# Optimization experiments

Measured on AMD Instinct MI355X. Metric: run time of the kernel, lower is better.

Reference implementation:

```python
import jax, jax.numpy as jnp
import numpy as np

B, S, D_IN, D_OUT, RANK, HBS, ABS = 4, 2048, 4096, 4096, 32, 128, 16


def _hadamard(n: int) -> np.ndarray:
    H = np.array([[1.0]], dtype=np.float64)
    while H.shape[0] < n:
        H = np.block([[H, H], [H, -H]])
    return (H / np.sqrt(n)).astype(np.float32)


def setup_inputs() -> dict:
    key = jax.random.key(0)
    ks = jax.random.split(key, 6)
    x = jax.random.normal(ks[0], (B, S, D_IN), dtype=jnp.float32)
    # random +/-1 sign vector (matches torch.randint(0,2)*2-1)
    S_in = (jax.random.randint(ks[1], (D_IN,), 0, 2) * 2 - 1).astype(jnp.float32)
    H_block = jnp.asarray(_hadamard(HBS))  # orthonormal block Hadamard
    w_quantized = jax.random.normal(ks[2], (D_OUT, D_IN), dtype=jnp.float32) * 0.02
    lora_a = jax.random.normal(ks[3], (RANK, D_IN), dtype=jnp.float32) * 0.01
    lora_b = jax.random.normal(ks[4], (D_OUT, RANK), dtype=jnp.float32) * 0.01
    bias = jax.random.normal(ks[5], (D_OUT,), dtype=jnp.float32) * 0.01
    return {"x": x, "S_in": S_in, "H_block": H_block, "w_quantized": w_quantized,
            "lora_a": lora_a, "lora_b": lora_b, "bias": bias}


def _quantize_nvfp4(x, block_size=ABS):
    # per-block (size 16) NVFP4 fake-quant; numel here is divisible by block_size
    levels = jnp.array([0.0, 0.5, 1.0, 1.5, 2.0, 3.0, 4.0, 6.0], dtype=x.dtype)
    shape = x.shape
    xf = x.reshape(-1, block_size)
    amax = jnp.maximum(jnp.max(jnp.abs(xf), axis=-1, keepdims=True), 1e-12)
    scale = amax / 6.0
    x_norm = jnp.abs(xf) / scale
    idx = jnp.argmin(jnp.abs(x_norm[..., None] - levels), axis=-1)  # snap to grid
    xq = jnp.sign(xf) * levels[idx] * scale
    return xq.reshape(shape)


def _hadamard_rotate(x, S_in, H_block):
    # sign flip then block-diagonal Hadamard on the last dim
    shape = x.shape
    x_s = x * S_in
    x3 = x_s.reshape(*shape[:-1], shape[-1] // HBS, HBS)
    return (x3 @ H_block).reshape(shape)


def reference(x, S_in, H_block, w_quantized, lora_a, lora_b, bias):
    x_rot = _hadamard_rotate(x, S_in, H_block)          # [B,S,D_IN]
    x_q = _quantize_nvfp4(x_rot)                        # NVFP4 fake-quant activations
    out = jnp.einsum('bsd,od->bso', x_q, w_quantized)   # main GEMM
    # LoRA correction on the (unquantized) rotated activations
    out = out + jnp.einsum('bsr,or->bso', jnp.einsum('bsd,rd->bsr', x_rot, lora_a), lora_b)
    out = out + bias
    return out
```

## Files before the change

kernel.cpp:

```cpp
#include <hip/hip_runtime.h>

#define M_ROWS 8192
#define DIN    4096
#define DOUT   4096
#define RANK   32
#define KAUG   4128
#define KPAD   4160
#define KTILES 65
#define ROWS_PB 4

typedef __attribute__((ext_vector_type(8))) short short8;
typedef __attribute__((ext_vector_type(4))) float floatx4;

__device__ __forceinline__ unsigned short f2bf(float f) {
    unsigned int u = __float_as_uint(f);
    unsigned int r = (u + 0x7FFFu + ((u >> 16) & 1u)) >> 16;
    return (unsigned short)r;
}

__global__ __launch_bounds__(256) void rot_quant_kernel(
    const float* __restrict__ x, const float* __restrict__ sgn,
    const float* __restrict__ lora_a, unsigned short* __restrict__ xaug)
{
    __shared__ unsigned short xrot[ROWS_PB][DIN];
    __shared__ float tred[ROWS_PB][RANK][8];

    const int t = threadIdx.x;
    const int row0 = blockIdx.x * ROWS_PB;
    const float inv = 0.08838834764831845f;

    float sg[16];
    #pragma unroll
    for (int q = 0; q < 4; ++q)
        *(float4*)&sg[4 * q] = ((const float4*)sgn)[t * 4 + q];

    if (t < ROWS_PB * 4) {
        const int rr = t >> 2, q = t & 3;
        *(uint4*)&xaug[(size_t)(row0 + rr) * KPAD + KAUG + q * 8] =
            make_uint4(0, 0, 0, 0);
    }

    #pragma unroll 1
    for (int rr = 0; rr < ROWS_PB; ++rr) {
        const float* xr = x + (size_t)(row0 + rr) * DIN;
        float v[16];
        #pragma unroll
        for (int q = 0; q < 4; ++q)
            *(float4*)&v[4 * q] = ((const float4*)xr)[t * 4 + q];
        #pragma unroll
        for (int j = 0; j < 16; ++j) v[j] *= sg[j];

        #pragma unroll
        for (int h = 1; h < 16; h <<= 1) {
            #pragma unroll
            for (int i = 0; i < 16; ++i) {
                if (!(i & h)) {
                    float a = v[i], b = v[i + h];
                    v[i] = a + b;
                    v[i + h] = a - b;
                }
            }
        }
        #pragma unroll
        for (int m = 1; m <= 4; m <<= 1) {
            const bool up = (t & m) != 0;
            #pragma unroll
            for (int j = 0; j < 16; ++j) {
                float o = __shfl_xor(v[j], m, 64);
                v[j] = up ? (o - v[j]) : (v[j] + o);
            }
        }
        #pragma unroll
        for (int j = 0; j < 16; ++j) v[j] *= inv;

        {
            unsigned int xp[8];
            #pragma unroll
            for (int j = 0; j < 8; ++j)
                xp[j] = (unsigned int)f2bf(v[2 * j]) |
                        ((unsigned int)f2bf(v[2 * j + 1]) << 16);
            *(uint4*)&xrot[rr][16 * t]     = make_uint4(xp[0], xp[1], xp[2], xp[3]);
            *(uint4*)&xrot[rr][16 * t + 8] = make_uint4(xp[4], xp[5], xp[6], xp[7]);
        }

        {
            float amax = 0.f;
            #pragma unroll
            for (int j = 0; j < 16; ++j) amax = fmaxf(amax, fabsf(v[j]));
            amax = fmaxf(amax, 1e-12f);
            float scale = amax / 6.0f;
            unsigned int pk[8];
            #pragma unroll
            for (int j = 0; j < 8; ++j) {
                unsigned short q2[2];
                #pragma unroll
                for (int e = 0; e < 2; ++e) {
                    float vv = v[2 * j + e];
                    float an = fabsf(vv) / scale;
                    float lev = 0.0f;
                    lev = an > 0.25f ? 0.5f : lev;
                    lev = an > 0.75f ? 1.0f : lev;
                    lev = an > 1.25f ? 1.5f : lev;
                    lev = an > 1.75f ? 2.0f : lev;
                    lev = an > 2.5f  ? 3.0f : lev;
                    lev = an > 3.5f  ? 4.0f : lev;
                    lev = an > 5.0f  ? 6.0f : lev;
                    q2[e] = f2bf(copysignf(lev * scale, vv));
                }
                pk[j] = (unsigned int)q2[0] | ((unsigned int)q2[1] << 16);
            }
            unsigned short* orow = xaug + (size_t)(row0 + rr) * KPAD + 16 * t;
            ((uint4*)orow)[0] = make_uint4(pk[0], pk[1], pk[2], pk[3]);
            ((uint4*)orow)[1] = make_uint4(pk[4], pk[5], pk[6], pk[7]);
        }
    }
    __syncthreads();

    {
        const int r = t >> 3, c = t & 7;
        const float* ar = lora_a + (size_t)r * DIN;
        float acc4[ROWS_PB] = {0.f, 0.f, 0.f, 0.f};
        #pragma unroll 1
        for (int i = 0; i < 64; ++i) {
            const int d = (c << 9) + (((i << 3) + (c << 3)) & 511);
            float4 a0 = *(const float4*)(ar + d);
            float4 a1 = *(const float4*)(ar + d + 4);
            #pragma unroll
            for (int rr = 0; rr < ROWS_PB; ++rr) {
                uint4 xb = *(const uint4*)&xrot[rr][d];
                float x0 = __uint_as_float(xb.x << 16);
                float x1 = __uint_as_float(xb.x & 0xFFFF0000u);
                float x2 = __uint_as_float(xb.y << 16);
                float x3 = __uint_as_float(xb.y & 0xFFFF0000u);
                float x4 = __uint_as_float(xb.z << 16);
                float x5 = __uint_as_float(xb.z & 0xFFFF0000u);
                float x6 = __uint_as_float(xb.w << 16);
                float x7 = __uint_as_float(xb.w & 0xFFFF0000u);
                acc4[rr] += a0.x * x0 + a0.y * x1 + a0.z * x2 + a0.w * x3 +
                            a1.x * x4 + a1.y * x5 + a1.z * x6 + a1.w * x7;
            }
        }
        #pragma unroll
        for (int rr = 0; rr < ROWS_PB; ++rr) tred[rr][r][c] = acc4[rr];
    }
    __syncthreads();
    if (t < ROWS_PB * RANK) {
        const int rr = t >> 5, rk = t & 31;
        float s = 0.f;
        #pragma unroll
        for (int k = 0; k < 8; ++k) s += tred[rr][rk][k];
        xaug[(size_t)(row0 + rr) * KPAD + DIN + rk] = f2bf(s);
    }
}

__global__ __launch_bounds__(256) void cast_w_kernel(
    const float* __restrict__ w, const float* __restrict__ lora_b,
    unsigned short* __restrict__ waug)
{
    const int n = blockIdx.x;
    const int t = threadIdx.x;
    unsigned short* wr = waug + (size_t)n * KPAD;
    const float* wsrc = w + (size_t)n * DIN;
    #pragma unroll
    for (int it = 0; it < 2; ++it) {
        const int base = (it * 256 + t) * 8;
        float4 a = ((const float4*)wsrc)[base >> 2];
        float4 b = ((const float4*)wsrc)[(base >> 2) + 1];
        unsigned int p0 = (unsigned int)f2bf(a.x) | ((unsigned int)f2bf(a.y) << 16);
        unsigned int p1 = (unsigned int)f2bf(a.z) | ((unsigned int)f2bf(a.w) << 16);
        unsigned int p2 = (unsigned int)f2bf(b.x) | ((unsigned int)f2bf(b.y) << 16);
        unsigned int p3 = (unsigned int)f2bf(b.z) | ((unsigned int)f2bf(b.w) << 16);
        *(uint4*)(wr + base) = make_uint4(p0, p1, p2, p3);
    }
    if (t < RANK)
        wr[DIN + t] = f2bf(lora_b[(size_t)n * RANK + t]);
    if (t < 4)
        *(uint4*)&wr[KAUG + t * 8] = make_uint4(0, 0, 0, 0);
}

__global__ __launch_bounds__(512) void gemm_kernel(
    const unsigned short* __restrict__ A,
    const unsigned short* __restrict__ Bm,
    const float* __restrict__ bias,
    float* __restrict__ C)
{
    __shared__ unsigned short As[2][256 * 64];
    __shared__ unsigned short Bs[2][256 * 64];

    const int bid = blockIdx.x;
    const int mt = bid >> 4, nt = bid & 15;
    const int m0 = mt * 256, n0 = nt * 256;
    const int t = threadIdx.x;
    const int wave = t >> 6, lane = t & 63;
    const int wm = wave >> 2, wn = wave & 3;
    const int lm = lane & 15, lq = lane >> 4;

    const int sr = lane >> 3;
    const int ss = (lane & 7) ^ sr;
    const int ca = wave * 4;

#define STAGE_A(buf, kt, c) do {                                              \
    const unsigned short* g_ = A + (size_t)(m0 + (c) * 8 + sr) * KPAD         \
                                 + (kt) * 64 + ss * 8;                        \
    __builtin_amdgcn_global_load_lds(                                         \
        (const __attribute__((address_space(1))) void*)g_,                    \
        (__attribute__((address_space(3))) void*)(&As[buf][(c) * 512]),       \
        16, 0, 0); } while (0)
#define STAGE_B(buf, kt, c) do {                                              \
    const unsigned short* g_ = Bm + (size_t)(n0 + (c) * 8 + sr) * KPAD        \
                                 + (kt) * 64 + ss * 8;                        \
    __builtin_amdgcn_global_load_lds(                                         \
        (const __attribute__((address_space(1))) void*)g_,                    \
        (__attribute__((address_space(3))) void*)(&Bs[buf][(c) * 512]),       \
        16, 0, 0); } while (0)

    const int cb0 = (lq * 16) ^ ((lm & 7) << 4);
    const int cb1 = (64 + lq * 16) ^ ((lm & 7) << 4);
    const int arow = (wm * 128 + lm) * 128;
    const int brow = (wn * 64 + lm) * 128;

    floatx4 acc[8][4] = {};

    STAGE_A(0, 0, ca + 0); STAGE_A(0, 0, ca + 1);
    STAGE_A(0, 0, ca + 2); STAGE_A(0, 0, ca + 3);
    STAGE_B(0, 0, ca + 0); STAGE_B(0, 0, ca + 1);
    STAGE_B(0, 0, ca + 2); STAGE_B(0, 0, ca + 3);

    for (int kt = 0; kt < KTILES; ++kt) {
        const int b = kt & 1;
        const char* as = (const char*)&As[b][0];
        const char* bs = (const char*)&Bs[b][0];
        short8 af[4], bf[4];

        if (kt + 1 < KTILES) {
            STAGE_A(b ^ 1, kt + 1, ca + 0);
            STAGE_A(b ^ 1, kt + 1, ca + 1);
            asm volatile("s_waitcnt vmcnt(2)" ::: "memory");
        } else {
            asm volatile("s_waitcnt vmcnt(0)" ::: "memory");
        }
        __builtin_amdgcn_s_barrier();
        #pragma unroll
        for (int i = 0; i < 4; ++i)
            af[i] = *(const short8*)(as + arow + i * 2048 + cb0);
        #pragma unroll
        for (int j = 0; j < 4; ++j)
            bf[j] = *(const short8*)(bs + brow + j * 2048 + cb0);
        __builtin_amdgcn_s_setprio(1);
        #pragma unroll
        for (int i = 0; i < 4; ++i)
            #pragma unroll
            for (int j = 0; j < 4; ++j)
                acc[i][j] = __builtin_amdgcn_mfma_f32_16x16x32_bf16(
                    af[i], bf[j], acc[i][j], 0, 0, 0);
        __builtin_amdgcn_s_setprio(0);
        __builtin_amdgcn_s_barrier();

        #pragma unroll
        for (int i = 0; i < 4; ++i)
            af[i] = *(const short8*)(as + arow + (i + 4) * 2048 + cb0);
        if (kt + 1 < KTILES) {
            STAGE_A(b ^ 1, kt + 1, ca + 2);
            STAGE_A(b ^ 1, kt + 1, ca + 3);
        }
        __builtin_amdgcn_s_barrier();
        __builtin_amdgcn_s_setprio(1);
        #pragma unroll
        for (int i = 0; i < 4; ++i)
            #pragma unroll
            for (int j = 0; j < 4; ++j)
                acc[i + 4][j] = __builtin_amdgcn_mfma_f32_16x16x32_bf16(
                    af[i], bf[j], acc[i + 4][j], 0, 0, 0);
        __builtin_amdgcn_s_setprio(0);
        __builtin_amdgcn_s_barrier();

        #pragma unroll
        for (int i = 0; i < 4; ++i)
            af[i] = *(const short8*)(as + arow + i * 2048 + cb1);
        #pragma unroll
        for (int j = 0; j < 4; ++j)
            bf[j] = *(const short8*)(bs + brow + j * 2048 + cb1);
        if (kt + 1 < KTILES) {
            STAGE_B(b ^ 1, kt + 1, ca + 0);
            STAGE_B(b ^ 1, kt + 1, ca + 1);
        }
        __builtin_amdgcn_s_barrier();
        __builtin_amdgcn_s_setprio(1);
        #pragma unroll
        for (int i = 0; i < 4; ++i)
            #pragma unroll
            for (int j = 0; j < 4; ++j)
                acc[i][j] = __builtin_amdgcn_mfma_f32_16x16x32_bf16(
                    af[i], bf[j], acc[i][j], 0, 0, 0);
        __builtin_amdgcn_s_setprio(0);
        __builtin_amdgcn_s_barrier();

        #pragma unroll
        for (int i = 0; i < 4; ++i)
            af[i] = *(const short8*)(as + arow + (i + 4) * 2048 + cb1);
        if (kt + 1 < KTILES) {
            STAGE_B(b ^ 1, kt + 1, ca + 2);
            STAGE_B(b ^ 1, kt + 1, ca + 3);
        }
        __builtin_amdgcn_s_barrier();
        __builtin_amdgcn_s_setprio(1);
        #pragma unroll
        for (int i = 0; i < 4; ++i)
            #pragma unroll
            for (int j = 0; j < 4; ++j)
                acc[i + 4][j] = __builtin_amdgcn_mfma_f32_16x16x32_bf16(
                    af[i], bf[j], acc[i + 4][j], 0, 0, 0);
        __builtin_amdgcn_s_setprio(0);
        __builtin_amdgcn_s_barrier();
    }

    float bv[4];
    #pragma unroll
    for (int j = 0; j < 4; ++j)
        bv[j] = bias[n0 + wn * 64 + j * 16 + lm];
    #pragma unroll
    for (int i = 0; i < 8; ++i) {
        #pragma unroll
        for (int j = 0; j < 4; ++j) {
            const int col = n0 + wn * 64 + j * 16 + lm;
            #pragma unroll
            for (int r = 0; r < 4; ++r) {
                const int row = m0 + wm * 128 + i * 16 + lq * 4 + r;
                C[(size_t)row * DOUT + col] = acc[i][j][r] + bv[j];
            }
        }
    }
#undef STAGE_A
#undef STAGE_B
}

extern "C" void kernel_launch(void* const* d_in, const int* in_sizes, int n_in,
                              void* d_out, int out_size, void* d_ws, size_t ws_size,
                              hipStream_t stream) {
    const float* x      = (const float*)d_in[0];
    const float* sgn    = (const float*)d_in[1];
    const float* w      = (const float*)d_in[3];
    const float* lora_a = (const float*)d_in[4];
    const float* lora_b = (const float*)d_in[5];
    const float* bias   = (const float*)d_in[6];
    float* out = (float*)d_out;

    unsigned short* xaug = (unsigned short*)d_ws;
    unsigned short* waug = xaug + (size_t)M_ROWS * KPAD;

    rot_quant_kernel<<<M_ROWS / ROWS_PB, 256, 0, stream>>>(x, sgn, lora_a, xaug);
    cast_w_kernel<<<DOUT, 256, 0, stream>>>(w, lora_b, waug);
    gemm_kernel<<<(M_ROWS / 256) * (DOUT / 256), 512, 0, stream>>>(xaug, waug, bias, out);
}
```

Baseline: 688.5 us.

## Merge prep kernels and restructure GEMM LDS staging into half-K sub-tiles

Folds the weight cast into the rotation/quant kernel as extra blocks, removing one launch and letting both prep workloads run concurrently. The GEMM now splits each 64-wide K tile into two 32-wide halves, each stored in its own LDS buffer with a 16-row by 4-segment XOR swizzle. Loads for the next tile are issued in quarter steps, with vmcnt waits placed so each half becomes ready just before it is used, and sched_barriers keep the compiler from reordering around the barriers. The aim is to cut LDS bank conflicts and per-tile synchronisation stalls. The risk is that the tighter wait pattern and changed layout could expose load latency or break correctness if the counts are off.

```diff
diff --git a/kernel.cpp b/kernel.cpp
--- a/kernel.cpp
+++ b/kernel.cpp
@@ -8,6 +8,7 @@
 #define KPAD   4160
 #define KTILES 65
 #define ROWS_PB 4
+#define NROTB  (M_ROWS / ROWS_PB)
 
 typedef __attribute__((ext_vector_type(8))) short short8;
 typedef __attribute__((ext_vector_type(4))) float floatx4;
@@ -18,14 +19,39 @@
     return (unsigned short)r;
 }
 
-__global__ __launch_bounds__(256) void rot_quant_kernel(
+__global__ __launch_bounds__(256) void prep_kernel(
     const float* __restrict__ x, const float* __restrict__ sgn,
-    const float* __restrict__ lora_a, unsigned short* __restrict__ xaug)
+    const float* __restrict__ lora_a,
+    const float* __restrict__ w, const float* __restrict__ lora_b,
+    unsigned short* __restrict__ xaug, unsigned short* __restrict__ waug)
 {
     __shared__ unsigned short xrot[ROWS_PB][DIN];
     __shared__ float tred[ROWS_PB][RANK][8];
 
     const int t = threadIdx.x;
+
+    if (blockIdx.x >= NROTB) {
+        const int n = blockIdx.x - NROTB;
+        unsigned short* wr = waug + (size_t)n * KPAD;
+        const float* wsrc = w + (size_t)n * DIN;
+        #pragma unroll
+        for (int it = 0; it < 2; ++it) {
+            const int base = (it * 256 + t) * 8;
+            float4 a = ((const float4*)wsrc)[base >> 2];
+            float4 b = ((const float4*)wsrc)[(base >> 2) + 1];
+            unsigned int p0 = (unsigned int)f2bf(a.x) | ((unsigned int)f2bf(a.y) << 16);
+            unsigned int p1 = (unsigned int)f2bf(a.z) | ((unsigned int)f2bf(a.w) << 16);
+            unsigned int p2 = (unsigned int)f2bf(b.x) | ((unsigned int)f2bf(b.y) << 16);
+            unsigned int p3 = (unsigned int)f2bf(b.z) | ((unsigned int)f2bf(b.w) << 16);
+            *(uint4*)(wr + base) = make_uint4(p0, p1, p2, p3);
+        }
+        if (t < RANK)
+            wr[DIN + t] = f2bf(lora_b[(size_t)n * RANK + t]);
+        if (t < 4)
+            *(uint4*)&wr[KAUG + t * 8] = make_uint4(0, 0, 0, 0);
+        return;
+    }
+
     const int row0 = blockIdx.x * ROWS_PB;
     const float inv = 0.08838834764831845f;
 
@@ -153,39 +179,14 @@
     }
 }
 
-__global__ __launch_bounds__(256) void cast_w_kernel(
-    const float* __restrict__ w, const float* __restrict__ lora_b,
-    unsigned short* __restrict__ waug)
-{
-    const int n = blockIdx.x;
-    const int t = threadIdx.x;
-    unsigned short* wr = waug + (size_t)n * KPAD;
-    const float* wsrc = w + (size_t)n * DIN;
-    #pragma unroll
-    for (int it = 0; it < 2; ++it) {
-        const int base = (it * 256 + t) * 8;
-        float4 a = ((const float4*)wsrc)[base >> 2];
-        float4 b = ((const float4*)wsrc)[(base >> 2) + 1];
-        unsigned int p0 = (unsigned int)f2bf(a.x) | ((unsigned int)f2bf(a.y) << 16);
-        unsigned int p1 = (unsigned int)f2bf(a.z) | ((unsigned int)f2bf(a.w) << 16);
-        unsigned int p2 = (unsigned int)f2bf(b.x) | ((unsigned int)f2bf(b.y) << 16);
-        unsigned int p3 = (unsigned int)f2bf(b.z) | ((unsigned int)f2bf(b.w) << 16);
-        *(uint4*)(wr + base) = make_uint4(p0, p1, p2, p3);
-    }
-    if (t < RANK)
-        wr[DIN + t] = f2bf(lora_b[(size_t)n * RANK + t]);
-    if (t < 4)
-        *(uint4*)&wr[KAUG + t * 8] = make_uint4(0, 0, 0, 0);
-}
-
 __global__ __launch_bounds__(512) void gemm_kernel(
     const unsigned short* __restrict__ A,
     const unsigned short* __restrict__ Bm,
     const float* __restrict__ bias,
     float* __restrict__ C)
 {
-    __shared__ unsigned short As[2][256 * 64];
-    __shared__ unsigned short Bs[2][256 * 64];
+    __shared__ unsigned short As[2][2][8192];
+    __shared__ unsigned short Bs[2][2][8192];
 
     const int bid = blockIdx.x;
     const int mt = bid >> 4, nt = bid & 15;
@@ -195,57 +196,53 @@
     const int wm = wave >> 2, wn = wave & 3;
     const int lm = lane & 15, lq = lane >> 4;
 
-    const int sr = lane >> 3;
-    const int ss = (lane & 7) ^ sr;
-    const int ca = wave * 4;
-
-#define STAGE_A(buf, kt, c) do {                                              \
-    const unsigned short* g_ = A + (size_t)(m0 + (c) * 8 + sr) * KPAD         \
-                                 + (kt) * 64 + ss * 8;                        \
+    const int pr = lane >> 2;
+    const int sgs = (lane & 3) ^ (pr & 3);
+    const int cc0 = wave * 2, cc1 = wave * 2 + 1;
+
+    const int rdo = lm * 64 + ((lq ^ (lm & 3)) << 4);
+
+#define STG(MAT, RB, DST, KT, KH, CC) do {                                    \
+    const unsigned short* g_ = (MAT) + (size_t)((RB) + (CC) * 16 + pr) * KPAD \
+                               + (KT) * 64 + (KH) * 32 + sgs * 8;             \
     __builtin_amdgcn_global_load_lds(                                         \
         (const __attribute__((address_space(1))) void*)g_,                    \
-        (__attribute__((address_space(3))) void*)(&As[buf][(c) * 512]),       \
+        (__attribute__((address_space(3))) void*)((DST) + (CC) * 512),        \
         16, 0, 0); } while (0)
-#define STAGE_B(buf, kt, c) do {                                              \
-    const unsigned short* g_ = Bm + (size_t)(n0 + (c) * 8 + sr) * KPAD        \
-                                 + (kt) * 64 + ss * 8;                        \
-    __builtin_amdgcn_global_load_lds(                                         \
-        (const __attribute__((address_space(1))) void*)g_,                    \
-        (__attribute__((address_space(3))) void*)(&Bs[buf][(c) * 512]),       \
-        16, 0, 0); } while (0)
-
-    const int cb0 = (lq * 16) ^ ((lm & 7) << 4);
-    const int cb1 = (64 + lq * 16) ^ ((lm & 7) << 4);
-    const int arow = (wm * 128 + lm) * 128;
-    const int brow = (wn * 64 + lm) * 128;
 
     floatx4 acc[8][4] = {};
 
-    STAGE_A(0, 0, ca + 0); STAGE_A(0, 0, ca + 1);
-    STAGE_A(0, 0, ca + 2); STAGE_A(0, 0, ca + 3);
-    STAGE_B(0, 0, ca + 0); STAGE_B(0, 0, ca + 1);
-    STAGE_B(0, 0, ca + 2); STAGE_B(0, 0, ca + 3);
-
+    STG(A,  m0, &As[0][0][0], 0, 0, cc0); STG(A,  m0, &As[0][0][0], 0, 0, cc1);
+    STG(Bm, n0, &Bs[0][0][0], 0, 0, cc0); STG(Bm, n0, &Bs[0][0][0], 0, 0, cc1);
+    STG(A,  m0, &As[0][1][0], 0, 1, cc0); STG(A,  m0, &As[0][1][0], 0, 1, cc1);
+    STG(Bm, n0, &Bs[0][1][0], 0, 1, cc0); STG(Bm, n0, &Bs[0][1][0], 0, 1, cc1);
+    asm volatile("s_waitcnt vmcnt(4)" ::: "memory");
+    __builtin_amdgcn_s_barrier();
+
+    #pragma unroll 1
     for (int kt = 0; kt < KTILES; ++kt) {
         const int b = kt & 1;
-        const char* as = (const char*)&As[b][0];
-        const char* bs = (const char*)&Bs[b][0];
+        const bool st = (kt + 1 < KTILES);
+        const char* a0c = (const char*)&As[b][0][0];
+        const char* a1c = (const char*)&As[b][1][0];
+        const char* b0c = (const char*)&Bs[b][0][0];
+        const char* b1c = (const char*)&Bs[b][1][0];
+        unsigned short* nA0 = &As[b ^ 1][0][0];
+        unsigned short* nA1 = &As[b ^ 1][1][0];
+        unsigned short* nB0 = &Bs[b ^ 1][0][0];
+        unsigned short* nB1 = &Bs[b ^ 1][1][0];
         short8 af[4], bf[4];
 
-        if (kt + 1 < KTILES) {
-            STAGE_A(b ^ 1, kt + 1, ca + 0);
-            STAGE_A(b ^ 1, kt + 1, ca + 1);
-            asm volatile("s_waitcnt vmcnt(2)" ::: "memory");
-        } else {
-            asm volatile("s_waitcnt vmcnt(0)" ::: "memory");
-        }
-        __builtin_amdgcn_s_barrier();
-        #pragma unroll
-        for (int i = 0; i < 4; ++i)
-            af[i] = *(const short8*)(as + arow + i * 2048 + cb0);
+        #pragma unroll
+        for (int i = 0; i < 4; ++i)
+            af[i] = *(const short8*)(a0c + (wm * 8 + i) * 1024 + rdo);
         #pragma unroll
         for (int j = 0; j < 4; ++j)
-            bf[j] = *(const short8*)(bs + brow + j * 2048 + cb0);
+            bf[j] = *(const short8*)(b0c + (wn * 4 + j) * 1024 + rdo);
+        if (st) { STG(A, m0, nA0, kt + 1, 0, cc0); STG(A, m0, nA0, kt + 1, 0, cc1); }
+        __builtin_amdgcn_sched_barrier(0);
+        __builtin_amdgcn_s_barrier();
+        __builtin_amdgcn_sched_barrier(0);
         __builtin_amdgcn_s_setprio(1);
         #pragma unroll
         for (int i = 0; i < 4; ++i)
@@ -254,16 +251,21 @@
                 acc[i][j] = __builtin_amdgcn_mfma_f32_16x16x32_bf16(
                     af[i], bf[j], acc[i][j], 0, 0, 0);
         __builtin_amdgcn_s_setprio(0);
-        __builtin_amdgcn_s_barrier();
-
-        #pragma unroll
-        for (int i = 0; i < 4; ++i)
-            af[i] = *(const short8*)(as + arow + (i + 4) * 2048 + cb0);
-        if (kt + 1 < KTILES) {
-            STAGE_A(b ^ 1, kt + 1, ca + 2);
-            STAGE_A(b ^ 1, kt + 1, ca + 3);
-        }
-        __builtin_amdgcn_s_barrier();
+        __builtin_amdgcn_sched_barrier(0);
+        __builtin_amdgcn_s_barrier();
+
+        #pragma unroll
+        for (int i = 0; i < 4; ++i)
+            af[i] = *(const short8*)(a0c + (wm * 8 + 4 + i) * 1024 + rdo);
+        if (st) {
+            STG(Bm, n0, nB0, kt + 1, 0, cc0); STG(Bm, n0, nB0, kt + 1, 0, cc1);
+            asm volatile("s_waitcnt vmcnt(4)" ::: "memory");
+        } else {
+            asm volatile("s_waitcnt vmcnt(0)" ::: "memory");
+        }
+        __builtin_amdgcn_sched_barrier(0);
+        __builtin_amdgcn_s_barrier();
+        __builtin_amdgcn_sched_barrier(0);
         __builtin_amdgcn_s_setprio(1);
         #pragma unroll
         for (int i = 0; i < 4; ++i)
@@ -272,19 +274,19 @@
                 acc[i + 4][j] = __builtin_amdgcn_mfma_f32_16x16x32_bf16(
                     af[i], bf[j], acc[i + 4][j], 0, 0, 0);
         __builtin_amdgcn_s_setprio(0);
-        __builtin_amdgcn_s_barrier();
-
-        #pragma unroll
-        for (int i = 0; i < 4; ++i)
-            af[i] = *(const short8*)(as + arow + i * 2048 + cb1);
+        __builtin_amdgcn_sched_barrier(0);
+        __builtin_amdgcn_s_barrier();
+
+        #pragma unroll
+        for (int i = 0; i < 4; ++i)
+            af[i] = *(const short8*)(a1c + (wm * 8 + i) * 1024 + rdo);
         #pragma unroll
         for (int j = 0; j < 4; ++j)
-            bf[j] = *(const short8*)(bs + brow + j * 2048 + cb1);
-        if (kt + 1 < KTILES) {
-            STAGE_B(b ^ 1, kt + 1, ca + 0);
-            STAGE_B(b ^ 1, kt + 1, ca + 1);
-        }
-        __builtin_amdgcn_s_barrier();
+            bf[j] = *(const short8*)(b1c + (wn * 4 + j) * 1024 + rdo);
+        if (st) { STG(A, m0, nA1, kt + 1, 1, cc0); STG(A, m0, nA1, kt + 1, 1, cc1); }
+        __builtin_amdgcn_sched_barrier(0);
+        __builtin_amdgcn_s_barrier();
+        __builtin_amdgcn_sched_barrier(0);
         __builtin_amdgcn_s_setprio(1);
         #pragma unroll
         for (int i = 0; i < 4; ++i)
@@ -293,16 +295,19 @@
                 acc[i][j] = __builtin_amdgcn_mfma_f32_16x16x32_bf16(
                     af[i], bf[j], acc[i][j], 0, 0, 0);
         __builtin_amdgcn_s_setprio(0);
-        __builtin_amdgcn_s_barrier();
-
-        #pragma unroll
-        for (int i = 0; i < 4; ++i)
-            af[i] = *(const short8*)(as + arow + (i + 4) * 2048 + cb1);
-        if (kt + 1 < KTILES) {
-            STAGE_B(b ^ 1, kt + 1, ca + 2);
-            STAGE_B(b ^ 1, kt + 1, ca + 3);
-        }
-        __builtin_amdgcn_s_barrier();
+        __builtin_amdgcn_sched_barrier(0);
+        __builtin_amdgcn_s_barrier();
+
+        #pragma unroll
+        for (int i = 0; i < 4; ++i)
+            af[i] = *(const short8*)(a1c + (wm * 8 + 4 + i) * 1024 + rdo);
+        if (st) {
+            STG(Bm, n0, nB1, kt + 1, 1, cc0); STG(Bm, n0, nB1, kt + 1, 1, cc1);
+            asm volatile("s_waitcnt vmcnt(4)" ::: "memory");
+        }
+        __builtin_amdgcn_sched_barrier(0);
+        __builtin_amdgcn_s_barrier();
+        __builtin_amdgcn_sched_barrier(0);
         __builtin_amdgcn_s_setprio(1);
         #pragma unroll
         for (int i = 0; i < 4; ++i)
@@ -311,8 +316,10 @@
                 acc[i + 4][j] = __builtin_amdgcn_mfma_f32_16x16x32_bf16(
                     af[i], bf[j], acc[i + 4][j], 0, 0, 0);
         __builtin_amdgcn_s_setprio(0);
-        __builtin_amdgcn_s_barrier();
-    }
+        __builtin_amdgcn_sched_barrier(0);
+        __builtin_amdgcn_s_barrier();
+    }
+#undef STG
 
     float bv[4];
     #pragma unroll
@@ -330,8 +337,6 @@
             }
         }
     }
-#undef STAGE_A
-#undef STAGE_B
 }
 
 extern "C" void kernel_launch(void* const* d_in, const int* in_sizes, int n_in,
@@ -348,7 +353,7 @@
     unsigned short* xaug = (unsigned short*)d_ws;
     unsigned short* waug = xaug + (size_t)M_ROWS * KPAD;
 
-    rot_quant_kernel<<<M_ROWS / ROWS_PB, 256, 0, stream>>>(x, sgn, lora_a, xaug);
-    cast_w_kernel<<<DOUT, 256, 0, stream>>>(w, lora_b, waug);
+    prep_kernel<<<NROTB + DOUT, 256, 0, stream>>>(x, sgn, lora_a, w, lora_b,
+                                                  xaug, waug);
     gemm_kernel<<<(M_ROWS / 256) * (DOUT / 256), 512, 0, stream>>>(xaug, waug, bias, out);
 }
```

Measured after the change: 650.3 us. -5.5%, faster.
